# Performance work log

Hardware: AMD Instinct MI355X
Metric: run time of the kernel (lower is better)

Reference implementation:

```python
import jax, jax.numpy as jnp
import numpy as np

C = 256
CI = C // 2  # inter_channels
EPS = 1e-5


def _proj(x, w, b):
    # 1x1 conv == channel matmul: w [O,C], x [n,c,h,w] -> [n,o,h,w]
    return jnp.einsum('oc,nchw->nohw', w, x) + b[None, :, None, None]


def setup_inputs() -> dict:
    key = jax.random.key(0)
    ks = jax.random.split(key, 12)
    shp = (4, C, 64, 64)
    s = 1.0 / np.sqrt(C)
    si = 1.0 / np.sqrt(CI)
    return {
        'x': jax.random.normal(ks[0], shp, jnp.float32),
        'y': jax.random.normal(ks[1], shp, jnp.float32),
        'theta_w': jax.random.normal(ks[2], (CI, C), jnp.float32) * s,
        'theta_b': jax.random.normal(ks[3], (CI,), jnp.float32) * s,
        'phi_w': jax.random.normal(ks[4], (CI, C), jnp.float32) * s,
        'phi_b': jax.random.normal(ks[5], (CI,), jnp.float32) * s,
        'g_w': jax.random.normal(ks[6], (CI, C), jnp.float32) * s,
        'g_b': jax.random.normal(ks[7], (CI,), jnp.float32) * s,
        'rec_w': jax.random.normal(ks[8], (C, CI), jnp.float32) * si,
        'rec_b': jax.random.normal(ks[9], (C,), jnp.float32) * si,
        'gamma': jnp.ones((C,), jnp.float32),
        'beta': jnp.zeros((C,), jnp.float32),
    }


def reference(x, y, theta_w, theta_b, phi_w, phi_b, g_w, g_b, rec_w, rec_b, gamma, beta):
    n, c, h, w = x.shape
    hw = h * w
    # projections (1x1 convs)
    g_x = _proj(x, g_w, g_b).reshape(n, CI, hw).transpose(0, 2, 1)        # [n,HW,CI]
    theta_x = _proj(x, theta_w, theta_b).reshape(n, CI, hw).transpose(0, 2, 1)  # [n,HW,CI]
    phi_y = _proj(y, phi_w, phi_b).reshape(n, CI, hw)                     # [n,CI,HW]
    # attention: QK^T -> softmax -> AV
    attn = jax.nn.softmax(jnp.einsum('nqc,nck->nqk', theta_x, phi_y), axis=-1)  # [n,HW,HW]
    out = jnp.einsum('nqk,nkc->nqc', attn, g_x)                           # [n,HW,CI]
    out = out.transpose(0, 2, 1).reshape(n, CI, h, w)
    out = _proj(out, rec_w, rec_b)                                        # [n,C,h,w]
    # BatchNorm2d (training-mode forward: batch stats over N,H,W; biased var)
    mean = out.mean(axis=(0, 2, 3))
    var = out.var(axis=(0, 2, 3))
    out = gamma[None, :, None, None] * (out - mean[None, :, None, None]) * jax.lax.rsqrt(var + EPS)[None, :, None, None] + beta[None, :, None, None]
    return x + out
```

## Files before the change

### kernel.cpp

```cpp
#include <hip/hip_runtime.h>
#include <math.h>

#define EPSV 1e-5f

typedef __attribute__((ext_vector_type(8))) _Float16 f16x8;
typedef __attribute__((ext_vector_type(4))) _Float16 f16x4;
typedef __attribute__((ext_vector_type(4))) float f32x4;

typedef __attribute__((address_space(1))) const unsigned int as1_u32;
typedef __attribute__((address_space(3))) unsigned int as3_u32;

static __device__ __forceinline__ unsigned packh2(float a, float b) {
  auto v = __builtin_amdgcn_cvt_pkrtz(a, b);
  return __builtin_bit_cast(unsigned, v);
}

__global__ __launch_bounds__(256) void pack_xy(
    const float* __restrict__ x, const float* __restrict__ y,
    const float* __restrict__ tw, const float* __restrict__ pw,
    const float* __restrict__ gw, const float* __restrict__ rw,
    _Float16* __restrict__ xt, _Float16* __restrict__ w16) {
  if (blockIdx.z == 2) {
    int i = (blockIdx.y * 512 + blockIdx.x) * 256 + threadIdx.x;
    if (i < 131072) {
      const float* s = i < 32768 ? tw : (i < 65536 ? pw : (i < 98304 ? gw : rw));
      w16[i] = (_Float16)s[i & 32767];
    }
    return;
  }
  const int n = blockIdx.y, s = blockIdx.z;
  const int g = blockIdx.x * 256 + threadIdx.x;
  const int p = g & 4095, c8 = g >> 12;
  const float* src = (s ? y : x) + ((size_t)n * 256 + c8 * 8) * 4096 + p;
  f16x8 v;
#pragma unroll
  for (int j = 0; j < 8; ++j) v[j] = (_Float16)src[(size_t)j * 4096];
  *(f16x8*)(xt + ((size_t)(s * 4 + n) * 4096 + p) * 256 + c8 * 8) = v;
}

__global__ __launch_bounds__(256) void proj_kernel(
    const _Float16* __restrict__ xt, const _Float16* __restrict__ w16,
    const float* __restrict__ tb, const float* __restrict__ pb,
    const float* __restrict__ gb, _Float16* __restrict__ th16,
    _Float16* __restrict__ ph16, _Float16* __restrict__ g16) {
  const int ptile = blockIdx.x;
  const int z = blockIdx.y;
  const int pr = z >> 2, n = z & 3;
  const int p0 = ptile * 64;
  const int tid = threadIdx.x, wv = tid >> 6, lane = tid & 63, lg = lane >> 4, lr = lane & 15;

  __shared__ __align__(16) char sB[32768];

  const int srcn = (pr == 1 ? 4 : 0) + n;
  const char* src = (const char*)(xt + ((size_t)srcn * 4096 + p0) * 256);
#pragma unroll
  for (int ps = 0; ps < 8; ++ps) {
    int L = ps * 4096 + tid * 16;
    int row = L >> 9, col = L & 511;
    __builtin_amdgcn_global_load_lds((as1_u32*)(src + (size_t)row * 512 + (col ^ ((row & 7) << 4))),
                                     (as3_u32*)(sB + L), 16, 0, 0);
  }
  const _Float16* wp = w16 + pr * 32768;
  const float* bp = pr == 0 ? tb : (pr == 1 ? pb : gb);

  if (pr == 2) {
    const int o0 = wv * 32;
    f16x8 a[2][8];
#pragma unroll
    for (int mf = 0; mf < 2; ++mf)
#pragma unroll
      for (int kc = 0; kc < 8; ++kc)
        a[mf][kc] = *(const f16x8*)(wp + (size_t)(o0 + mf * 16 + lr) * 256 + kc * 32 + lg * 8);
    __syncthreads();
    f32x4 acc[2][4];
#pragma unroll
    for (int mf = 0; mf < 2; ++mf)
#pragma unroll
      for (int nf = 0; nf < 4; ++nf) acc[mf][nf] = f32x4{0.f, 0.f, 0.f, 0.f};
#pragma unroll
    for (int kc = 0; kc < 8; ++kc) {
      f16x8 bf[4];
#pragma unroll
      for (int nf = 0; nf < 4; ++nf)
        bf[nf] = *(const f16x8*)(sB + (nf * 16 + lr) * 512 + ((kc * 64 + lg * 16) ^ ((lr & 7) << 4)));
#pragma unroll
      for (int mf = 0; mf < 2; ++mf)
#pragma unroll
        for (int nf = 0; nf < 4; ++nf)
          acc[mf][nf] = __builtin_amdgcn_mfma_f32_16x16x32_f16(a[mf][kc], bf[nf], acc[mf][nf], 0, 0, 0);
    }
    _Float16* out = g16 + (size_t)n * 524288;
#pragma unroll
    for (int mf = 0; mf < 2; ++mf)
#pragma unroll
      for (int r = 0; r < 4; ++r) {
        int o = o0 + mf * 16 + lg * 4 + r;
        float bias = bp[o];
#pragma unroll
        for (int nf = 0; nf < 4; ++nf) {
          int pp = p0 + nf * 16 + lr;
          out[(size_t)((pp >> 5) * 128 + o) * 32 + (pp & 31)] = (_Float16)(acc[mf][nf][r] + bias);
        }
      }
  } else {
    __syncthreads();
    f32x4 acc[8];
#pragma unroll
    for (int nf = 0; nf < 8; ++nf) acc[nf] = f32x4{0.f, 0.f, 0.f, 0.f};
#pragma unroll 2
    for (int kc = 0; kc < 8; ++kc) {
      f16x8 bf[8];
#pragma unroll
      for (int nf = 0; nf < 8; ++nf)
        bf[nf] = *(const f16x8*)(wp + (size_t)(nf * 16 + lr) * 256 + kc * 32 + lg * 8);
      f16x8 af = *(const f16x8*)(sB + (wv * 16 + lr) * 512 + ((kc * 64 + lg * 16) ^ ((lr & 7) << 4)));
#pragma unroll
      for (int nf = 0; nf < 8; ++nf)
        acc[nf] = __builtin_amdgcn_mfma_f32_16x16x32_f16(af, bf[nf], acc[nf], 0, 0, 0);
    }
    _Float16* out = (pr == 0 ? th16 : ph16) + (size_t)n * 4096 * 128;
#pragma unroll
    for (int r = 0; r < 4; ++r) {
      int p = p0 + wv * 16 + lg * 4 + r;
#pragma unroll
      for (int nf = 0; nf < 8; ++nf) {
        int o = nf * 16 + lr;
        out[(size_t)p * 128 + o] = (_Float16)(acc[nf][r] + bp[o]);
      }
    }
  }
}

__global__ __launch_bounds__(256, 2) void attn_kernel(
    const _Float16* __restrict__ th16, const _Float16* __restrict__ ph16,
    const _Float16* __restrict__ g16, _Float16* __restrict__ po16,
    float2* __restrict__ ml) {
  const int lin = blockIdx.x;
  const int xcd = lin & 7;
  const int n = xcd >> 1;
  const int kvh = xcd & 1;
  const int rest = lin >> 3;
  const int qt = rest >> 1;
  const int kvq = kvh * 2 + (rest & 1);
  const int q0 = qt * 128;
  const int tid = threadIdx.x;
  const int wv = tid >> 6, lane = tid & 63, lg = lane >> 4, lr = lane & 15;
  const int kv0 = kvq * 1024;

  __shared__ __align__(16) char smem[40960];
#define KBUF(B) (smem + (B) * 8192)
#define GBUF(B) (smem + 16384 + (B) * 8192)
  char* pB = smem + 32768 + wv * 2048;

  const _Float16* thn = th16 + (size_t)n * 4096 * 128;
  const char* phn = (const char*)(ph16 + (size_t)n * 4096 * 128);
  const char* ggn = (const char*)(g16 + (size_t)n * 524288);

  const char* ksrc = phn + (size_t)kv0 * 256 + (tid >> 4) * 256 +
                     (((tid & 15) * 16) ^ (((tid >> 4) & 7) << 4));
  const char* gsrc = ggn + (size_t)kvq * 262144 + (tid >> 2) * 64 +
                     (((tid & 3) * 16) ^ (((tid >> 3) & 3) << 4));

#define STAGE(KT, B)                                                                     \
  do {                                                                                   \
    const char* ks = ksrc + (size_t)(KT) * 8192;                                         \
    const char* gs = gsrc + (size_t)(KT) * 8192;                                         \
    char* kd = KBUF(B) + tid * 16;                                                       \
    char* gd = GBUF(B) + tid * 16;                                                       \
    __builtin_amdgcn_global_load_lds((as1_u32*)ks, (as3_u32*)kd, 16, 0, 0);              \
    __builtin_amdgcn_global_load_lds((as1_u32*)(ks + 4096), (as3_u32*)(kd + 4096), 16, 0, 0); \
    __builtin_amdgcn_global_load_lds((as1_u32*)gs, (as3_u32*)gd, 16, 0, 0);              \
    __builtin_amdgcn_global_load_lds((as1_u32*)(gs + 4096), (as3_u32*)(gd + 4096), 16, 0, 0); \
  } while (0)

  f16x8 qf[2][4];
#pragma unroll
  for (int qg = 0; qg < 2; ++qg)
#pragma unroll
    for (int ch = 0; ch < 4; ++ch)
      qf[qg][ch] = *(const f16x8*)(thn + (size_t)(q0 + wv * 32 + qg * 16 + lr) * 128 +
                                   ch * 32 + lg * 8);

  const int swzk = (lr & 7) << 4;
  const int swzg = ((lr >> 1) & 3) << 4;
  const int swzp = ((lr >> 1) & 3) << 4;

  f32x4 acc[2][8];
#pragma unroll
  for (int qg = 0; qg < 2; ++qg)
#pragma unroll
    for (int of = 0; of < 8; ++of) acc[qg][of] = f32x4{0.f, 0.f, 0.f, 0.f};
  float m[2] = {-INFINITY, -INFINITY};
  float lrow[2] = {0.f, 0.f};

  STAGE(0, 0);
  __syncthreads();

  for (int kt = 0; kt < 32; ++kt) {
    const int b = kt & 1;
    if (kt < 31) STAGE(kt + 1, b ^ 1);

    const char* kb = KBUF(b);
    f32x4 s[2][2];
#pragma unroll
    for (int cf = 0; cf < 2; ++cf) {
      s[cf][0] = f32x4{0.f, 0.f, 0.f, 0.f};
      s[cf][1] = f32x4{0.f, 0.f, 0.f, 0.f};
    }
    __builtin_amdgcn_s_setprio(1);
#pragma unroll
    for (int cf = 0; cf < 2; ++cf) {
      const char* krow = kb + (cf * 16 + lr) * 256;
#pragma unroll
      for (int ch = 0; ch < 4; ++ch) {
        f16x8 kf = *(const f16x8*)(krow + ((ch * 64 + lg * 16) ^ swzk));
        s[cf][0] = __builtin_amdgcn_mfma_f32_16x16x32_f16(kf, qf[0][ch], s[cf][0], 0, 0, 0);
        s[cf][1] = __builtin_amdgcn_mfma_f32_16x16x32_f16(kf, qf[1][ch], s[cf][1], 0, 0, 0);
      }
    }
    __builtin_amdgcn_s_setprio(0);

    float mt0 = fmaxf(fmaxf(fmaxf(s[0][0][0], s[0][0][1]), fmaxf(s[0][0][2], s[0][0][3])),
                      fmaxf(fmaxf(s[1][0][0], s[1][0][1]), fmaxf(s[1][0][2], s[1][0][3])));
    float mt1 = fmaxf(fmaxf(fmaxf(s[0][1][0], s[0][1][1]), fmaxf(s[0][1][2], s[0][1][3])),
                      fmaxf(fmaxf(s[1][1][0], s[1][1][1]), fmaxf(s[1][1][2], s[1][1][3])));
    bool ok = (mt0 <= m[0] + 8.0f) && (mt1 <= m[1] + 8.0f);
    if (!__all(ok)) {
      mt0 = fmaxf(mt0, __shfl_xor(mt0, 16)); mt0 = fmaxf(mt0, __shfl_xor(mt0, 32));
      mt1 = fmaxf(mt1, __shfl_xor(mt1, 16)); mt1 = fmaxf(mt1, __shfl_xor(mt1, 32));
      float mn0 = fmaxf(m[0], mt0), mn1 = fmaxf(m[1], mt1);
      float sc0 = __expf(m[0] - mn0), sc1 = __expf(m[1] - mn1);
#pragma unroll
      for (int of = 0; of < 8; ++of) { acc[0][of] *= sc0; acc[1][of] *= sc1; }
      lrow[0] *= sc0; lrow[1] *= sc1;
      m[0] = mn0; m[1] = mn1;
    }
#pragma unroll
    for (int qg = 0; qg < 2; ++qg) {
      char* prow = pB + qg * 1024 + lr * 64;
      float psum = 0.f;
#pragma unroll
      for (int cf = 0; cf < 2; ++cf) {
        float p0 = __expf(s[cf][qg][0] - m[qg]);
        float p1 = __expf(s[cf][qg][1] - m[qg]);
        float p2 = __expf(s[cf][qg][2] - m[qg]);
        float p3 = __expf(s[cf][qg][3] - m[qg]);
        psum += (p0 + p1) + (p2 + p3);
        unsigned long long w = (unsigned long long)packh2(p0, p1) |
                               ((unsigned long long)packh2(p2, p3) << 32);
        *(unsigned long long*)(prow + ((cf * 32 + lg * 8) ^ swzp)) = w;
      }
      lrow[qg] += psum;
    }

    const char* gb = GBUF(b);
    f16x8 pf0 = *(const f16x8*)(pB + lr * 64 + ((lg * 16) ^ swzp));
    f16x8 pf1 = *(const f16x8*)(pB + 1024 + lr * 64 + ((lg * 16) ^ swzp));
    __builtin_amdgcn_s_setprio(1);
#pragma unroll
    for (int of = 0; of < 8; ++of) {
      f16x8 gf = *(const f16x8*)(gb + (of * 16 + lr) * 64 + ((lg * 16) ^ swzg));
      acc[0][of] = __builtin_amdgcn_mfma_f32_16x16x32_f16(gf, pf0, acc[0][of], 0, 0, 0);
      acc[1][of] = __builtin_amdgcn_mfma_f32_16x16x32_f16(gf, pf1, acc[1][of], 0, 0, 0);
    }
    __builtin_amdgcn_s_setprio(0);
    __syncthreads();
  }

  float L0 = lrow[0];
  L0 += __shfl_xor(L0, 16); L0 += __shfl_xor(L0, 32);
  float L1 = lrow[1];
  L1 += __shfl_xor(L1, 16); L1 += __shfl_xor(L1, 32);

  float* ep = (float*)(smem + wv * 8448);
#pragma unroll
  for (int qg = 0; qg < 2; ++qg) {
#pragma unroll
    for (int of = 0; of < 8; ++of)
#pragma unroll
      for (int r = 0; r < 4; ++r) ep[lr * 132 + of * 16 + lg * 4 + r] = acc[qg][of][r];
    char* pon = (char*)(po16 + ((size_t)(kvq * 4 + n) * 4096 + q0 + wv * 32 + qg * 16) * 128);
#pragma unroll
    for (int it = 0; it < 4; ++it) {
      int e = lane + it * 64;
      int qq = e >> 4, c8 = e & 15;
      f32x4 va = *(const f32x4*)(ep + qq * 132 + c8 * 8);
      f32x4 vb = *(const f32x4*)(ep + qq * 132 + c8 * 8 + 4);
      f16x8 h;
#pragma unroll
      for (int j = 0; j < 4; ++j) { h[j] = (_Float16)va[j]; h[4 + j] = (_Float16)vb[j]; }
      *(f16x8*)(pon + (size_t)qq * 256 + c8 * 16) = h;
    }
    if (lg == 0)
      ml[(size_t)(kvq * 4 + n) * 4096 + q0 + wv * 32 + qg * 16 + lr] =
          float2{m[qg], qg == 0 ? L0 : L1};
  }
#undef STAGE
#undef KBUF
#undef GBUF
}

__global__ __launch_bounds__(256) void rec_kernel(
    const _Float16* __restrict__ po16, const float2* __restrict__ ml,
    const _Float16* __restrict__ rw16, const float* __restrict__ rb,
    _Float16* __restrict__ rec16, float* __restrict__ partial) {
  const int pblk = blockIdx.x;
  const int n = blockIdx.y;
  const int p0 = pblk * 32;
  const int blin = n * 128 + pblk;
  const int tid = threadIdx.x, wv = tid >> 6, lane = tid & 63, lg = lane >> 4, lr = lane & 15;
  __shared__ __align__(16) char sB[8192];

  {
    const int row = tid >> 3;
    const int c0 = (tid & 7) * 16;
    float2 v[4];
    float M = -INFINITY;
#pragma unroll
    for (int k = 0; k < 4; ++k) {
      v[k] = ml[(size_t)(k * 4 + n) * 4096 + p0 + row];
      M = fmaxf(M, v[k].x);
    }
    float f[4], L = 0.f;
#pragma unroll
    for (int k = 0; k < 4; ++k) {
      f[k] = __expf(v[k].x - M);
      L += v[k].y * f[k];
    }
    const float inv = 1.0f / L;
    float o[16];
#pragma unroll
    for (int j = 0; j < 16; ++j) o[j] = 0.f;
#pragma unroll
    for (int k = 0; k < 4; ++k) {
      const _Float16* p = po16 + ((size_t)(k * 4 + n) * 4096 + p0 + row) * 128 + c0;
      f16x8 a = *(const f16x8*)p;
      f16x8 b = *(const f16x8*)(p + 8);
#pragma unroll
      for (int j = 0; j < 8; ++j) {
        o[j] += f[k] * (float)a[j];
        o[8 + j] += f[k] * (float)b[j];
      }
    }
    f16x8 h0, h1;
#pragma unroll
    for (int j = 0; j < 8; ++j) {
      h0[j] = (_Float16)(o[j] * inv);
      h1[j] = (_Float16)(o[8 + j] * inv);
    }
    char* dst = sB + row * 256;
    const int xr = (row & 7) << 4;
    *(f16x8*)(dst + ((c0 * 2) ^ xr)) = h0;
    *(f16x8*)(dst + ((c0 * 2 + 16) ^ xr)) = h1;
  }

  const int wc0 = wv * 64;
  f16x8 a[4][4];
#pragma unroll
  for (int mf = 0; mf < 4; ++mf)
#pragma unroll
    for (int kc = 0; kc < 4; ++kc)
      a[mf][kc] = *(const f16x8*)(rw16 + (size_t)(wc0 + mf * 16 + lr) * 128 + kc * 32 + lg * 8);
  __syncthreads();

  f32x4 acc[4][2];
#pragma unroll
  for (int mf = 0; mf < 4; ++mf) {
    acc[mf][0] = f32x4{0.f, 0.f, 0.f, 0.f};
    acc[mf][1] = f32x4{0.f, 0.f, 0.f, 0.f};
  }
  const int xorv = (lr & 7) << 4;
#pragma unroll
  for (int kc = 0; kc < 4; ++kc) {
    int cb = (kc * 64 + lg * 16) ^ xorv;
    f16x8 b0 = *(const f16x8*)(sB + lr * 256 + cb);
    f16x8 b1 = *(const f16x8*)(sB + (16 + lr) * 256 + cb);
#pragma unroll
    for (int mf = 0; mf < 4; ++mf) {
      acc[mf][0] = __builtin_amdgcn_mfma_f32_16x16x32_f16(a[mf][kc], b0, acc[mf][0], 0, 0, 0);
      acc[mf][1] = __builtin_amdgcn_mfma_f32_16x16x32_f16(a[mf][kc], b1, acc[mf][1], 0, 0, 0);
    }
  }
  float* pslot = partial + (size_t)blin * 512;
#pragma unroll
  for (int mf = 0; mf < 4; ++mf)
#pragma unroll
    for (int r = 0; r < 4; ++r) {
      int c = wc0 + mf * 16 + lg * 4 + r;
      float bias = rb[c];
      float v0 = acc[mf][0][r] + bias;
      float v1 = acc[mf][1][r] + bias;
      rec16[((size_t)n * 256 + c) * 4096 + p0 + lr] = (_Float16)v0;
      rec16[((size_t)n * 256 + c) * 4096 + p0 + 16 + lr] = (_Float16)v1;
      float s = v0 + v1, qd = v0 * v0 + v1 * v1;
      s += __shfl_xor(s, 1); qd += __shfl_xor(qd, 1);
      s += __shfl_xor(s, 2); qd += __shfl_xor(qd, 2);
      s += __shfl_xor(s, 4); qd += __shfl_xor(qd, 4);
      s += __shfl_xor(s, 8); qd += __shfl_xor(qd, 8);
      if (lr == 0) {
        pslot[c] = s;
        pslot[256 + c] = qd;
      }
    }
}

__global__ __launch_bounds__(256) void stats_reduce(const float* __restrict__ partial,
                                                    float* __restrict__ stats) {
  const int tid = threadIdx.x;
  const int j = blockIdx.x * 32 + (tid >> 3);
  const int sub = tid & 7;
  float s = 0.f;
#pragma unroll 8
  for (int i = 0; i < 64; ++i) s += partial[(size_t)(i * 8 + sub) * 512 + j];
  s += __shfl_xor(s, 1);
  s += __shfl_xor(s, 2);
  s += __shfl_xor(s, 4);
  if (sub == 0) stats[j] = s;
}

__global__ __launch_bounds__(256) void bn_kernel(
    const float* __restrict__ x, const float* __restrict__ gamma,
    const float* __restrict__ beta, const float* __restrict__ stats,
    const _Float16* __restrict__ rec16, float* __restrict__ out) {
  const size_t i4 = (size_t)blockIdx.x * 256 + threadIdx.x;
  const int c = (int)((i4 >> 10) & 255);
  const float inv = 1.f / 16384.f;
  const float mean = stats[c] * inv;
  const float var = stats[256 + c] * inv - mean * mean;
  const float gm = gamma[c] * rsqrtf(var + EPSV);
  const float bt = beta[c];
  f16x4 r4 = ((const f16x4*)rec16)[i4];
  float4 xv = ((const float4*)x)[i4];
  float4 o;
  o.x = xv.x + ((float)r4[0] - mean) * gm + bt;
  o.y = xv.y + ((float)r4[1] - mean) * gm + bt;
  o.z = xv.z + ((float)r4[2] - mean) * gm + bt;
  o.w = xv.w + ((float)r4[3] - mean) * gm + bt;
  ((float4*)out)[i4] = o;
}

extern "C" void kernel_launch(void* const* d_in, const int* in_sizes, int n_in,
                              void* d_out, int out_size, void* d_ws, size_t ws_size,
                              hipStream_t stream) {
  const float* x  = (const float*)d_in[0];
  const float* y  = (const float*)d_in[1];
  const float* tw = (const float*)d_in[2];
  const float* tb = (const float*)d_in[3];
  const float* pw = (const float*)d_in[4];
  const float* pb = (const float*)d_in[5];
  const float* gw = (const float*)d_in[6];
  const float* gb = (const float*)d_in[7];
  const float* rw = (const float*)d_in[8];
  const float* rb = (const float*)d_in[9];
  const float* gamma = (const float*)d_in[10];
  const float* beta  = (const float*)d_in[11];
  float* out = (float*)d_out;
  _Float16* xt    = (_Float16*)d_ws;
  _Float16* w16   = xt + 8388608;
  _Float16* th16  = w16 + 131072;
  _Float16* ph16  = th16 + 2097152;
  _Float16* g16   = ph16 + 2097152;
  _Float16* rec16 = g16 + 2097152;
  float* partial  = (float*)(rec16 + 4194304);
  float* stats    = partial + 262144;
  float2* ml      = (float2*)(stats + 512);
  _Float16* po16  = xt;
  _Float16* rw16 = w16 + 98304;
  pack_xy<<<dim3(512, 4, 3), 256, 0, stream>>>(x, y, tw, pw, gw, rw, xt, w16);
  proj_kernel<<<dim3(64, 12), 256, 0, stream>>>(xt, w16, tb, pb, gb, th16, ph16, g16);
  attn_kernel<<<dim3(512), 256, 0, stream>>>(th16, ph16, g16, po16, ml);
  rec_kernel<<<dim3(128, 4), 256, 0, stream>>>(po16, ml, rw16, rb, rec16, partial);
  stats_reduce<<<dim3(16), 256, 0, stream>>>(partial, stats);
  bn_kernel<<<dim3(4096), 256, 0, stream>>>(x, gamma, beta, stats, rec16, out);
}
```

Measured before the change: 116.1 us.

## Split KV range across two wave halves in attention block with register-staged loads

The attention kernel grows to 512 threads. Two groups of four waves each process half of every 64-key tile for the same 128 queries, and their partial softmax states (max, sum, accumulators) are merged through LDS at the end. Async global-to-LDS double buffering is replaced by register staging: each thread loads the next tile into registers while the current one is computed, then writes it to a single LDS buffer. The aim is more waves in flight to hide latency. The risks are the extra merge and barrier steps, and a tighter register budget from launch_bounds(512,4) that could cause spills.

```diff
diff --git a/kernel.cpp b/kernel.cpp
--- a/kernel.cpp
+++ b/kernel.cpp
@@ -131,7 +131,7 @@
   }
 }
 
-__global__ __launch_bounds__(256, 2) void attn_kernel(
+__global__ __launch_bounds__(512, 4) void attn_kernel(
     const _Float16* __restrict__ th16, const _Float16* __restrict__ ph16,
     const _Float16* __restrict__ g16, _Float16* __restrict__ po16,
     float2* __restrict__ ml) {
@@ -145,40 +145,45 @@
   const int q0 = qt * 128;
   const int tid = threadIdx.x;
   const int wv = tid >> 6, lane = tid & 63, lg = lane >> 4, lr = lane & 15;
+  const int qsub = wv & 3, half = wv >> 2;
   const int kv0 = kvq * 1024;
 
-  __shared__ __align__(16) char smem[40960];
-#define KBUF(B) (smem + (B) * 8192)
-#define GBUF(B) (smem + 16384 + (B) * 8192)
+  __shared__ __align__(16) char smem[49152];
   char* pB = smem + 32768 + wv * 2048;
 
   const _Float16* thn = th16 + (size_t)n * 4096 * 128;
   const char* phn = (const char*)(ph16 + (size_t)n * 4096 * 128);
   const char* ggn = (const char*)(g16 + (size_t)n * 524288);
 
-  const char* ksrc = phn + (size_t)kv0 * 256 + (tid >> 4) * 256 +
-                     (((tid & 15) * 16) ^ (((tid >> 4) & 7) << 4));
-  const char* gsrc = ggn + (size_t)kvq * 262144 + (tid >> 2) * 64 +
-                     (((tid & 3) * 16) ^ (((tid >> 3) & 3) << 4));
-
-#define STAGE(KT, B)                                                                     \
+  const int t2 = tid & 255;
+  const char* ksrc = phn + (size_t)kv0 * 256 + (t2 >> 4) * 256 +
+                     (((t2 & 15) * 16) ^ (((t2 >> 4) & 7) << 4));
+  const char* gsrc = ggn + (size_t)kvq * 262144 + (t2 >> 2) * 64 +
+                     (((t2 & 3) * 16) ^ (((t2 >> 3) & 3) << 4));
+  const char* src0 = (tid < 256) ? ksrc : gsrc;
+  char* dst0 = smem + (tid < 256 ? 0 : 16384) + t2 * 16;
+
+  f32x4 stg[4];
+
+#define LOADT(KT)                                                                        \
   do {                                                                                   \
-    const char* ks = ksrc + (size_t)(KT) * 8192;                                         \
-    const char* gs = gsrc + (size_t)(KT) * 8192;                                         \
-    char* kd = KBUF(B) + tid * 16;                                                       \
-    char* gd = GBUF(B) + tid * 16;                                                       \
-    __builtin_amdgcn_global_load_lds((as1_u32*)ks, (as3_u32*)kd, 16, 0, 0);              \
-    __builtin_amdgcn_global_load_lds((as1_u32*)(ks + 4096), (as3_u32*)(kd + 4096), 16, 0, 0); \
-    __builtin_amdgcn_global_load_lds((as1_u32*)gs, (as3_u32*)gd, 16, 0, 0);              \
-    __builtin_amdgcn_global_load_lds((as1_u32*)(gs + 4096), (as3_u32*)(gd + 4096), 16, 0, 0); \
+    const char* s_ = src0 + (size_t)(KT) * 16384;                                        \
+    _Pragma("unroll") for (int i_ = 0; i_ < 4; ++i_)                                     \
+        stg[i_] = *(const f32x4*)(s_ + i_ * 4096);                                       \
   } while (0)
 
+#define WRITET()                                                                         \
+  do {                                                                                   \
+    _Pragma("unroll") for (int i_ = 0; i_ < 4; ++i_)                                     \
+        *(f32x4*)(dst0 + i_ * 4096) = stg[i_];                                           \
+  } while (0)
+
   f16x8 qf[2][4];
 #pragma unroll
   for (int qg = 0; qg < 2; ++qg)
 #pragma unroll
     for (int ch = 0; ch < 4; ++ch)
-      qf[qg][ch] = *(const f16x8*)(thn + (size_t)(q0 + wv * 32 + qg * 16 + lr) * 128 +
+      qf[qg][ch] = *(const f16x8*)(thn + (size_t)(q0 + qsub * 32 + qg * 16 + lr) * 128 +
                                    ch * 32 + lg * 8);
 
   const int swzk = (lr & 7) << 4;
@@ -193,14 +198,12 @@
   float m[2] = {-INFINITY, -INFINITY};
   float lrow[2] = {0.f, 0.f};
 
-  STAGE(0, 0);
+  LOADT(0);
+  WRITET();
+  LOADT(1);
   __syncthreads();
 
-  for (int kt = 0; kt < 32; ++kt) {
-    const int b = kt & 1;
-    if (kt < 31) STAGE(kt + 1, b ^ 1);
-
-    const char* kb = KBUF(b);
+  for (int kt = 0; kt < 16; ++kt) {
     f32x4 s[2][2];
 #pragma unroll
     for (int cf = 0; cf < 2; ++cf) {
@@ -210,7 +213,7 @@
     __builtin_amdgcn_s_setprio(1);
 #pragma unroll
     for (int cf = 0; cf < 2; ++cf) {
-      const char* krow = kb + (cf * 16 + lr) * 256;
+      const char* krow = smem + (half * 32 + cf * 16 + lr) * 256;
 #pragma unroll
       for (int ch = 0; ch < 4; ++ch) {
         f16x8 kf = *(const f16x8*)(krow + ((ch * 64 + lg * 16) ^ swzk));
@@ -253,51 +256,84 @@
       lrow[qg] += psum;
     }
 
-    const char* gb = GBUF(b);
+    const char* gbh = smem + 16384 + half * 8192;
     f16x8 pf0 = *(const f16x8*)(pB + lr * 64 + ((lg * 16) ^ swzp));
     f16x8 pf1 = *(const f16x8*)(pB + 1024 + lr * 64 + ((lg * 16) ^ swzp));
     __builtin_amdgcn_s_setprio(1);
 #pragma unroll
     for (int of = 0; of < 8; ++of) {
-      f16x8 gf = *(const f16x8*)(gb + (of * 16 + lr) * 64 + ((lg * 16) ^ swzg));
+      f16x8 gf = *(const f16x8*)(gbh + (of * 16 + lr) * 64 + ((lg * 16) ^ swzg));
       acc[0][of] = __builtin_amdgcn_mfma_f32_16x16x32_f16(gf, pf0, acc[0][of], 0, 0, 0);
       acc[1][of] = __builtin_amdgcn_mfma_f32_16x16x32_f16(gf, pf1, acc[1][of], 0, 0, 0);
     }
     __builtin_amdgcn_s_setprio(0);
     __syncthreads();
-  }
-
-  float L0 = lrow[0];
-  L0 += __shfl_xor(L0, 16); L0 += __shfl_xor(L0, 32);
-  float L1 = lrow[1];
-  L1 += __shfl_xor(L1, 16); L1 += __shfl_xor(L1, 32);
-
-  float* ep = (float*)(smem + wv * 8448);
+    if (kt < 15) {
+      WRITET();
+      if (kt < 14) LOADT(kt + 2);
+      __syncthreads();
+    }
+  }
+
+  float Lq[2];
+  Lq[0] = lrow[0];
+  Lq[0] += __shfl_xor(Lq[0], 16); Lq[0] += __shfl_xor(Lq[0], 32);
+  Lq[1] = lrow[1];
+  Lq[1] += __shfl_xor(Lq[1], 16); Lq[1] += __shfl_xor(Lq[1], 32);
+
+  float mM[2], lM[2];
 #pragma unroll
   for (int qg = 0; qg < 2; ++qg) {
-#pragma unroll
-    for (int of = 0; of < 8; ++of)
-#pragma unroll
-      for (int r = 0; r < 4; ++r) ep[lr * 132 + of * 16 + lg * 4 + r] = acc[qg][of][r];
-    char* pon = (char*)(po16 + ((size_t)(kvq * 4 + n) * 4096 + q0 + wv * 32 + qg * 16) * 128);
-#pragma unroll
-    for (int it = 0; it < 4; ++it) {
-      int e = lane + it * 64;
-      int qq = e >> 4, c8 = e & 15;
-      f32x4 va = *(const f32x4*)(ep + qq * 132 + c8 * 8);
-      f32x4 vb = *(const f32x4*)(ep + qq * 132 + c8 * 8 + 4);
-      f16x8 h;
-#pragma unroll
-      for (int j = 0; j < 4; ++j) { h[j] = (_Float16)va[j]; h[4 + j] = (_Float16)vb[j]; }
-      *(f16x8*)(pon + (size_t)qq * 256 + c8 * 16) = h;
-    }
-    if (lg == 0)
-      ml[(size_t)(kvq * 4 + n) * 4096 + q0 + wv * 32 + qg * 16 + lr] =
-          float2{m[qg], qg == 0 ? L0 : L1};
-  }
-#undef STAGE
-#undef KBUF
-#undef GBUF
+    float* slot = (float*)smem + qsub * 2304;
+    if (half == 1) {
+      float* as = slot + lane * 36;
+#pragma unroll
+      for (int of = 0; of < 8; ++of) *(f32x4*)(as + of * 4) = acc[qg][of];
+      as[32] = m[qg];
+      as[33] = Lq[qg];
+    }
+    __syncthreads();
+    if (half == 0) {
+      const float* as = slot + lane * 36;
+      float pm = as[32], pl = as[33];
+      float mm = fmaxf(m[qg], pm);
+      float a0 = __expf(m[qg] - mm), a1 = __expf(pm - mm);
+#pragma unroll
+      for (int of = 0; of < 8; ++of)
+        acc[qg][of] = acc[qg][of] * a0 + (*(const f32x4*)(as + of * 4)) * a1;
+      mM[qg] = mm;
+      lM[qg] = Lq[qg] * a0 + pl * a1;
+    }
+    __syncthreads();
+  }
+
+  if (half == 0) {
+    float* ep = (float*)(smem + qsub * 8448);
+#pragma unroll
+    for (int qg = 0; qg < 2; ++qg) {
+#pragma unroll
+      for (int of = 0; of < 8; ++of)
+#pragma unroll
+        for (int r = 0; r < 4; ++r) ep[lr * 132 + of * 16 + lg * 4 + r] = acc[qg][of][r];
+      char* pon = (char*)(po16 + ((size_t)(kvq * 4 + n) * 4096 + q0 + qsub * 32 + qg * 16) * 128);
+#pragma unroll
+      for (int it = 0; it < 4; ++it) {
+        int e = lane + it * 64;
+        int qq = e >> 4, c8 = e & 15;
+        f32x4 va = *(const f32x4*)(ep + qq * 132 + c8 * 8);
+        f32x4 vb = *(const f32x4*)(ep + qq * 132 + c8 * 8 + 4);
+        f16x8 h;
+#pragma unroll
+        for (int j = 0; j < 4; ++j) { h[j] = (_Float16)va[j]; h[4 + j] = (_Float16)vb[j]; }
+        *(f16x8*)(pon + (size_t)qq * 256 + c8 * 16) = h;
+      }
+      if (lg == 0)
+        ml[(size_t)(kvq * 4 + n) * 4096 + q0 + qsub * 32 + qg * 16 + lr] =
+            float2{mM[qg], lM[qg]};
+    }
+  }
+#undef LOADT
+#undef WRITET
 }
 
 __global__ __launch_bounds__(256) void rec_kernel(
@@ -468,7 +504,7 @@
   _Float16* rw16 = w16 + 98304;
   pack_xy<<<dim3(512, 4, 3), 256, 0, stream>>>(x, y, tw, pw, gw, rw, xt, w16);
   proj_kernel<<<dim3(64, 12), 256, 0, stream>>>(xt, w16, tb, pb, gb, th16, ph16, g16);
-  attn_kernel<<<dim3(512), 256, 0, stream>>>(th16, ph16, g16, po16, ml);
+  attn_kernel<<<dim3(512), 512, 0, stream>>>(th16, ph16, g16, po16, ml);
   rec_kernel<<<dim3(128, 4), 256, 0, stream>>>(po16, ml, rw16, rb, rec16, partial);
   stats_reduce<<<dim3(16), 256, 0, stream>>>(partial, stats);
   bn_kernel<<<dim3(4096), 256, 0, stream>>>(x, gamma, beta, stats, rec16, out);
```

Measured after the change: 227.7 us. 96.1% more time.
